# Performance work log

Hardware: AMD Instinct MI355X
Metric: run time of the kernel (lower is better)

Reference implementation:

```python
import jax, jax.numpy as jnp
import numpy as np

NUM_HEADS = 16
ROPE_THETA = 10000.0


def _rope_cos_sin(seq_len, head_dim, dtype):
    # Llama rotary embedding: inv_freq over even dims, emb = cat(freqs, freqs)
    inv_freq = 1.0 / (ROPE_THETA ** (jnp.arange(0, head_dim, 2, dtype=jnp.float32) / head_dim))
    t = jnp.arange(seq_len, dtype=jnp.float32)
    freqs = jnp.outer(t, inv_freq)              # [S, hd/2]
    emb = jnp.concatenate([freqs, freqs], -1)   # [S, hd]
    return jnp.cos(emb).astype(dtype), jnp.sin(emb).astype(dtype)


def _rotate_half(x):
    h = x.shape[-1] // 2
    return jnp.concatenate([-x[..., h:], x[..., :h]], axis=-1)


def setup_inputs() -> dict:
    key = jax.random.key(0)
    ks = jax.random.split(key, 5)
    B, S, D = 1, 2048, 2048
    scale = 0.02
    return {
        "hidden_states": jax.random.normal(ks[0], (B, S, D), jnp.float32),
        "Wq": jax.random.normal(ks[1], (D, D), jnp.float32) * scale,
        "Wk": jax.random.normal(ks[2], (D, D), jnp.float32) * scale,
        "Wv": jax.random.normal(ks[3], (D, D), jnp.float32) * scale,
        "Wo": jax.random.normal(ks[4], (D, D), jnp.float32) * scale,
    }


def reference(hidden_states, Wq, Wk, Wv, Wo):
    B, S, D = hidden_states.shape
    H = NUM_HEADS
    hd = D // H
    sm_scale = 1.0 / np.sqrt(hd)

    # QKV projections (nn.Linear without bias: x @ W.T), kept in [B,S,H,hd]
    q = (hidden_states @ Wq.T).reshape(B, S, H, hd)
    k = (hidden_states @ Wk.T).reshape(B, S, H, hd)
    v = (hidden_states @ Wv.T).reshape(B, S, H, hd)

    # RoPE (offset=0, no kv cache)
    cos, sin = _rope_cos_sin(S, hd, hidden_states.dtype)
    cos = cos[None, :, None, :]  # [1,S,1,hd]
    sin = sin[None, :, None, :]
    q = q * cos + _rotate_half(q) * sin
    k = k * cos + _rotate_half(k) * sin

    # Causal self-attention (exact math of FlashSelfAttention(causal=True))
    scores = jnp.einsum("bshd,bthd->bhst", q, k) * sm_scale  # [B,H,S,S]
    causal = jnp.tril(jnp.ones((S, S), dtype=bool))
    scores = jnp.where(causal[None, None], scores, jnp.finfo(scores.dtype).min)
    probs = jax.nn.softmax(scores, axis=-1)
    attn = jnp.einsum("bhst,bthd->bshd", probs, v)           # [B,S,H,hd]

    # Output projection
    attn = attn.reshape(B, S, H * hd)
    return attn @ Wo.T
```

## Files before the change

kernel.cpp:

```cpp
#include <hip/hip_runtime.h>
#include <hip/hip_bf16.h>
#include <math.h>

#define S_LEN 2048
#define DMODEL 2048
#define NHEADS 16
#define HDIM 128

typedef __bf16 bf16x8 __attribute__((ext_vector_type(8)));
typedef float f32x4 __attribute__((ext_vector_type(4)));

__device__ __forceinline__ unsigned short f2b(float f) {
  union { float f; unsigned u; } c; c.f = f;
  unsigned r = (c.u + 0x7fffu + ((c.u >> 16) & 1u)) >> 16;
  return (unsigned short)r;
}
__device__ __forceinline__ float b2f(unsigned short b) {
  union { unsigned u; float f; } c; c.u = ((unsigned)b) << 16;
  return c.f;
}

__device__ __forceinline__ void gload_lds16(const unsigned short* g, unsigned short* l) {
  __builtin_amdgcn_global_load_lds(
      (__attribute__((address_space(1))) void*)(void*)g,
      (__attribute__((address_space(3))) void*)(void*)l, 16, 0, 0);
}

__global__ void cvt5_f32_bf16_k(const float* __restrict__ s0,
                                const float* __restrict__ s1,
                                const float* __restrict__ s2,
                                const float* __restrict__ s3,
                                const float* __restrict__ s4,
                                unsigned short* __restrict__ d0,
                                unsigned short* __restrict__ d1,
                                unsigned short* __restrict__ d2,
                                unsigned short* __restrict__ d3,
                                unsigned short* __restrict__ d4) {
  int gi = blockIdx.x * blockDim.x + threadIdx.x;
  int seg = gi >> 20;
  int i = (gi & 0xFFFFF) * 4;
  const float* src = (seg == 0) ? s0 : (seg == 1) ? s1 : (seg == 2) ? s2
                     : (seg == 3) ? s3 : s4;
  unsigned short* dst = (seg == 0) ? d0 : (seg == 1) ? d1 : (seg == 2) ? d2
                        : (seg == 3) ? d3 : d4;
  float4 v = *reinterpret_cast<const float4*>(src + i);
  ushort4 o;
  o.x = f2b(v.x); o.y = f2b(v.y); o.z = f2b(v.z); o.w = f2b(v.w);
  *reinterpret_cast<ushort4*>(dst + i) = o;
}

__global__ void rope_table_k(float* __restrict__ cs, float* __restrict__ sn) {
  int idx = blockIdx.x * blockDim.x + threadIdx.x;
  int s = idx >> 6, i = idx & 63;
  float inv = powf(10000.0f, -(float)(2 * i) / 128.0f);
  float a = (float)s * inv;
  cs[idx] = cosf(a);
  sn[idx] = sinf(a);
}

__global__ void rope_apply_k(unsigned short* __restrict__ q,
                             unsigned short* __restrict__ k,
                             const float* __restrict__ cs,
                             const float* __restrict__ sn) {
  int idx = blockIdx.x * blockDim.x + threadIdx.x;
  int i = idx & 63;
  int h = (idx >> 6) & (NHEADS - 1);
  int s = idx >> 10;
  size_t base = (size_t)s * DMODEL + h * HDIM;
  float c = cs[s * 64 + i], sv = sn[s * 64 + i];
  float q1 = b2f(q[base + i]), q2 = b2f(q[base + i + 64]);
  q[base + i]      = f2b(q1 * c - q2 * sv);
  q[base + i + 64] = f2b(q2 * c + q1 * sv);
  float k1 = b2f(k[base + i]), k2 = b2f(k[base + i + 64]);
  k[base + i]      = f2b(k1 * c - k2 * sv);
  k[base + i + 64] = f2b(k2 * c + k1 * sv);
}

__global__ __launch_bounds__(256) void transpose_bf16_k(
    const unsigned short* __restrict__ in, unsigned short* __restrict__ out) {
  __shared__ unsigned short tile[64][72];
  int bx = blockIdx.x, by = blockIdx.y;
  int t = threadIdx.x;
#pragma unroll
  for (int i = 0; i < 2; ++i) {
    int ch = i * 256 + t;
    int r = ch >> 3, c8 = ch & 7;
    bf16x8 v = *reinterpret_cast<const bf16x8*>(
        in + (size_t)(by * 64 + r) * DMODEL + bx * 64 + c8 * 8);
    *reinterpret_cast<bf16x8*>(&tile[r][c8 * 8]) = v;
  }
  __syncthreads();
#pragma unroll
  for (int i = 0; i < 2; ++i) {
    int ch = i * 256 + t;
    int c = ch >> 3, r8 = ch & 7;
    union { bf16x8 v; unsigned short u[8]; } w;
#pragma unroll
    for (int j = 0; j < 8; ++j) w.u[j] = tile[r8 * 8 + j][c];
    *reinterpret_cast<bf16x8*>(
        out + (size_t)(bx * 64 + c) * S_LEN + by * 64 + r8 * 8) = w.v;
  }
}


#define MIDBAR_SEQ()                                      \
  do {                                                    \
    asm volatile("" ::: "memory");                        \
    __builtin_amdgcn_s_barrier();                         \
    asm volatile("s_waitcnt lgkmcnt(0)" ::: "memory");    \
    __builtin_amdgcn_sched_barrier(0);                    \
    __builtin_amdgcn_s_setprio(1);                        \
  } while (0)

#define ENDBAR_SEQ()                                      \
  do {                                                    \
    __builtin_amdgcn_s_setprio(0);                        \
    asm volatile("" ::: "memory");                        \
    __builtin_amdgcn_s_barrier();                         \
    asm volatile("" ::: "memory");                        \
  } while (0)

#define READA(QM)                                                              \
  do {                                                                         \
    _Pragma("unroll") for (int j = 0; j < MQ; ++j)                             \
    _Pragma("unroll") for (int kk = 0; kk < 2; ++kk) {                         \
      int row = wm * (BM / 2) + ((QM) * MQ + j) * 16 + li;                     \
      int c = (kk * 4 + g) ^ (li & 7);                                         \
      af[j][kk] = *reinterpret_cast<const bf16x8*>(&As[cur][row * 64 + c * 8]);\
    }                                                                          \
  } while (0)

#define READB(BF, QN)                                                          \
  do {                                                                         \
    _Pragma("unroll") for (int jn = 0; jn < 2; ++jn)                           \
    _Pragma("unroll") for (int kk = 0; kk < 2; ++kk) {                         \
      int row = wn * 64 + ((QN) * 2 + jn) * 16 + li;                           \
      int c = (kk * 4 + g) ^ (li & 7);                                         \
      BF[jn][kk] = *reinterpret_cast<const bf16x8*>(&Bs[cur][row * 64 + c * 8]);\
    }                                                                          \
  } while (0)

#define QUAD(QM, QN, BF)                                                       \
  do {                                                                         \
    _Pragma("unroll") for (int j = 0; j < MQ; ++j)                             \
    _Pragma("unroll") for (int jn = 0; jn < 2; ++jn)                           \
    _Pragma("unroll") for (int kk = 0; kk < 2; ++kk)                           \
      acc[(QM) * MQ + j][(QN) * 2 + jn] =                                      \
          __builtin_amdgcn_mfma_f32_16x16x32_bf16(                             \
              af[j][kk], BF[jn][kk], acc[(QM) * MQ + j][(QN) * 2 + jn], 0, 0, 0);\
  } while (0)

template <int BM, bool OUT_F32>
__global__ __launch_bounds__(512, 2) void gemm_8ph_k(
    const unsigned short* __restrict__ A, const unsigned short* __restrict__ B0p,
    const unsigned short* __restrict__ B1p, const unsigned short* __restrict__ B2p,
    void* __restrict__ C0, void* __restrict__ C1, void* __restrict__ C2,
    int M, int N, int K) {
  constexpr int MQ = BM / 64;
  constexpr int MR = BM / 32;

  __shared__ unsigned short As[2][BM * 64];
  __shared__ unsigned short Bs[2][256 * 64];

  const unsigned short* Bp = (blockIdx.z == 0) ? B0p : (blockIdx.z == 1) ? B1p : B2p;
  void* Cout = (blockIdx.z == 0) ? C0 : (blockIdx.z == 1) ? C1 : C2;

  int nwg = gridDim.x, bid = blockIdx.x;
  int wg = (bid & 7) * (nwg >> 3) + (bid >> 3);
  int ntn = N >> 8;
  int tm = wg / ntn, tn = wg % ntn;
  int m0 = tm * BM, n0 = tn << 8;

  const int tid = threadIdx.x;
  const int wave = tid >> 6, lane = tid & 63;
  const int g = lane >> 4, li = lane & 15;
  const int wm = wave >> 2, wn = wave & 3;

  auto stageB = [&](int buf, int tt, int qn) {
#pragma unroll
    for (int i = 0; i < 2; ++i) {
      int j = i * 512 + tid;
      int piece = j >> 8, rowin = (j >> 3) & 31, c = j & 7;
      int row = piece * 64 + qn * 32 + rowin;
      gload_lds16(Bp + (size_t)(n0 + row) * K + tt * 64 + ((c ^ (row & 7)) * 8),
                  &Bs[buf][row * 64 + c * 8]);
    }
  };
  auto stageA = [&](int buf, int tt, int qm) {
#pragma unroll
    for (int i = 0; i < BM / 128; ++i) {
      int j = i * 512 + tid;
      int piece = j / (2 * BM);
      int rowin = (j >> 3) & (BM / 4 - 1);
      int c = j & 7;
      int row = piece * (BM / 2) + qm * (BM / 4) + rowin;
      gload_lds16(A + (size_t)(m0 + row) * K + tt * 64 + ((c ^ (row & 7)) * 8),
                  &As[buf][row * 64 + c * 8]);
    }
  };

  f32x4 acc[MR][4];
#pragma unroll
  for (int i = 0; i < MR; ++i)
#pragma unroll
    for (int j = 0; j < 4; ++j) acc[i][j] = (f32x4){0.f, 0.f, 0.f, 0.f};

  const int nK = K >> 6;

  stageB(0, 0, 0); stageA(0, 0, 0); stageB(0, 0, 1); stageA(0, 0, 1);
  stageB(1, 1, 0); stageA(1, 1, 0); stageB(1, 1, 1); stageA(1, 1, 1);
  if constexpr (BM == 256) asm volatile("s_waitcnt vmcnt(8)" ::: "memory");
  else                     asm volatile("s_waitcnt vmcnt(6)" ::: "memory");
  asm volatile("" ::: "memory");
  __builtin_amdgcn_s_barrier();
  asm volatile("" ::: "memory");

  for (int t = 0; t < nK; ++t) {
    int cur = t & 1;
    bool pf = (t + 2 < nK);
    bf16x8 af[MQ][2], bf0[2][2], bf1[2][2];
    READA(0);
    READB(bf0, 0);
    MIDBAR_SEQ();
    QUAD(0, 0, bf0);
    ENDBAR_SEQ();
    READB(bf1, 1);
    if (pf) { stageB(cur, t + 2, 0); stageA(cur, t + 2, 0); }
    MIDBAR_SEQ();
    QUAD(0, 1, bf1);
    ENDBAR_SEQ();
    READA(1);
    if (pf) stageB(cur, t + 2, 1);
    MIDBAR_SEQ();
    QUAD(1, 1, bf1);
    ENDBAR_SEQ();
    if (pf) {
      stageA(cur, t + 2, 1);
      if constexpr (BM == 256) asm volatile("s_waitcnt vmcnt(8)" ::: "memory");
      else                     asm volatile("s_waitcnt vmcnt(6)" ::: "memory");
    } else {
      asm volatile("s_waitcnt vmcnt(0)" ::: "memory");
    }
    MIDBAR_SEQ();
    QUAD(1, 0, bf0);
    ENDBAR_SEQ();
  }

#pragma unroll
  for (int m = 0; m < MR; ++m) {
#pragma unroll
    for (int n = 0; n < 4; ++n) {
      int row = m0 + wm * (BM / 2) + m * 16 + g * 4;
      int col = n0 + wn * 64 + n * 16 + li;
#pragma unroll
      for (int r = 0; r < 4; ++r) {
        if (OUT_F32)
          reinterpret_cast<float*>(Cout)[(size_t)(row + r) * N + col] = acc[m][n][r];
        else
          reinterpret_cast<unsigned short*>(Cout)[(size_t)(row + r) * N + col] =
              f2b(acc[m][n][r]);
      }
    }
  }
}

#undef MIDBAR_SEQ
#undef ENDBAR_SEQ
#undef READA
#undef READB
#undef QUAD

__global__ __launch_bounds__(256) void flash_attn_k(
    const unsigned short* __restrict__ q, const unsigned short* __restrict__ k,
    const unsigned short* __restrict__ vt, unsigned short* __restrict__ o) {
  __shared__ unsigned short Ks[2][64 * 128];
  __shared__ unsigned short Vs[2][128 * 64];
  __shared__ unsigned short Ps[4 * 16 * 72];

  int L = blockIdx.x + 16 * blockIdx.y;
  int xcd = L & 7, j = L >> 3;
  int h = 2 * xcd + (j & 1);
  int p = j >> 1;

  int t = threadIdx.x, wave = t >> 6, lane = t & 63;
  int g = lane >> 4, li = lane & 15;

  const unsigned short* vth = vt + (size_t)h * HDIM * S_LEN;
  const float sm = 0.08838834764831845f;
  const float L2E = 1.4426950408889634f;

  auto stage = [&](int buf, int kt) {
    int kv0 = kt * 64;
#pragma unroll
    for (int i = 0; i < 4; ++i) {
      int ch = i * 256 + t;
      int row = ch >> 4, c = ch & 15;
      int cs_ = c ^ (row & 7);
      gload_lds16(k + (size_t)(kv0 + row) * DMODEL + h * HDIM + cs_ * 8,
                  &Ks[buf][ch * 8]);
    }
#pragma unroll
    for (int i = 0; i < 4; ++i) {
      int ch = i * 256 + t;
      int row = ch >> 3, c = ch & 7;
      int cs_ = c ^ (row & 7);
      gload_lds16(vth + (size_t)row * S_LEN + kv0 + cs_ * 8,
                  &Vs[buf][ch * 8]);
    }
  };

  for (int seg = 0; seg < 2; ++seg) {
    int qt = seg ? (31 - p) : p;
    int nIter = qt + 1;
    int q0 = qt * 64;
    int qrow = q0 + wave * 16 + li;

    bf16x8 qf[4];
#pragma unroll
    for (int kb = 0; kb < 4; ++kb)
      qf[kb] = *reinterpret_cast<const bf16x8*>(
          q + (size_t)qrow * DMODEL + h * HDIM + kb * 32 + g * 8);

    f32x4 O[8];
#pragma unroll
    for (int db = 0; db < 8; ++db) O[db] = (f32x4){0.f, 0.f, 0.f, 0.f};
    float m_r[4], l_r[4];
#pragma unroll
    for (int r = 0; r < 4; ++r) { m_r[r] = -1e30f; l_r[r] = 0.f; }

    stage(0, 0);

    for (int it = 0; it < nIter; ++it) {
      int cur = it & 1;
      int kv0 = it * 64;
      if (it + 1 < nIter) {
        stage(cur ^ 1, it + 1);
        asm volatile("s_waitcnt vmcnt(8)" ::: "memory");
      } else {
        asm volatile("s_waitcnt vmcnt(0)" ::: "memory");
      }
      __builtin_amdgcn_s_barrier();
      asm volatile("" ::: "memory");

      f32x4 sf[4];
#pragma unroll
      for (int jb = 0; jb < 4; ++jb) sf[jb] = (f32x4){0.f, 0.f, 0.f, 0.f};
#pragma unroll
      for (int kb = 0; kb < 4; ++kb) {
#pragma unroll
        for (int jb = 0; jb < 4; ++jb) {
          int row = jb * 16 + li;
          int c = (kb * 4 + g) ^ (row & 7);
          bf16x8 kf = *reinterpret_cast<const bf16x8*>(&Ks[cur][row * 128 + c * 8]);
          sf[jb] = __builtin_amdgcn_mfma_f32_16x16x32_bf16(qf[kb], kf, sf[jb], 0, 0, 0);
        }
      }

      float sv[4][4];
      float pm[4] = {-1e30f, -1e30f, -1e30f, -1e30f};
#pragma unroll
      for (int jb = 0; jb < 4; ++jb) {
        int jcol = kv0 + jb * 16 + li;
#pragma unroll
        for (int r = 0; r < 4; ++r) {
          float x = sf[jb][r] * sm;
          int irow = q0 + wave * 16 + g * 4 + r;
          if (it == qt && jcol > irow) x = -1e30f;
          sv[jb][r] = x;
          pm[r] = fmaxf(pm[r], x);
        }
      }
#pragma unroll
      for (int r = 0; r < 4; ++r) {
        float x = pm[r];
        x = fmaxf(x, __shfl_xor(x, 1));
        x = fmaxf(x, __shfl_xor(x, 2));
        x = fmaxf(x, __shfl_xor(x, 4));
        x = fmaxf(x, __shfl_xor(x, 8));
        pm[r] = x;
      }
      float alpha[4], ls[4];
#pragma unroll
      for (int r = 0; r < 4; ++r) {
        float nm = fmaxf(m_r[r], pm[r]);
        alpha[r] = exp2f((m_r[r] - nm) * L2E);
        m_r[r] = nm;
        ls[r] = 0.f;
      }
#pragma unroll
      for (int jb = 0; jb < 4; ++jb) {
#pragma unroll
        for (int r = 0; r < 4; ++r) {
          float pv = exp2f((sv[jb][r] - m_r[r]) * L2E);
          ls[r] += pv;
          Ps[wave * 16 * 72 + (g * 4 + r) * 72 + jb * 16 + li] = f2b(pv);
        }
      }
#pragma unroll
      for (int r = 0; r < 4; ++r) {
        float x = ls[r];
        x += __shfl_xor(x, 1);
        x += __shfl_xor(x, 2);
        x += __shfl_xor(x, 4);
        x += __shfl_xor(x, 8);
        l_r[r] = l_r[r] * alpha[r] + x;
      }
#pragma unroll
      for (int db = 0; db < 8; ++db)
#pragma unroll
        for (int r = 0; r < 4; ++r) O[db][r] *= alpha[r];

#pragma unroll
      for (int ks = 0; ks < 2; ++ks) {
        bf16x8 pa = *reinterpret_cast<const bf16x8*>(
            Ps + wave * 16 * 72 + li * 72 + ks * 32 + g * 8);
#pragma unroll
        for (int db = 0; db < 8; ++db) {
          int row = db * 16 + li;
          int c = (ks * 4 + g) ^ (row & 7);
          bf16x8 vbf = *reinterpret_cast<const bf16x8*>(&Vs[cur][row * 64 + c * 8]);
          O[db] = __builtin_amdgcn_mfma_f32_16x16x32_bf16(pa, vbf, O[db], 0, 0, 0);
        }
      }
      __builtin_amdgcn_s_barrier();
      asm volatile("" ::: "memory");
    }

#pragma unroll
    for (int db = 0; db < 8; ++db) {
#pragma unroll
      for (int r = 0; r < 4; ++r) {
        int row = q0 + wave * 16 + g * 4 + r;
        o[(size_t)row * DMODEL + h * HDIM + db * 16 + li] = f2b(O[db][r] / l_r[r]);
      }
    }
  }
}

extern "C" void kernel_launch(void* const* d_in, const int* in_sizes, int n_in,
                              void* d_out, int out_size, void* d_ws, size_t ws_size,
                              hipStream_t stream) {
  const float* hs = (const float*)d_in[0];
  const float* Wq = (const float*)d_in[1];
  const float* Wk = (const float*)d_in[2];
  const float* Wv = (const float*)d_in[3];
  const float* Wo = (const float*)d_in[4];

  char* ws = (char*)d_ws;
  const size_t MB = 1024 * 1024;
  unsigned short* hs_b = (unsigned short*)(ws + 0 * MB);
  unsigned short* Wq_b = (unsigned short*)(ws + 8 * MB);
  unsigned short* Wk_b = (unsigned short*)(ws + 16 * MB);
  unsigned short* Wv_b = (unsigned short*)(ws + 24 * MB);
  unsigned short* Wo_b = (unsigned short*)(ws + 32 * MB);
  unsigned short* qb = (unsigned short*)(ws + 40 * MB);
  unsigned short* kb = (unsigned short*)(ws + 48 * MB);
  unsigned short* vb = (unsigned short*)(ws + 56 * MB);
  unsigned short* ab = (unsigned short*)(ws + 64 * MB);
  float* cs = (float*)(ws + 72 * MB);
  float* sn = (float*)(ws + 72 * MB + 512 * 1024);
  unsigned short* vtb = hs_b;

  cvt5_f32_bf16_k<<<(5 * 1024 * 1024) / 256, 256, 0, stream>>>(
      hs, Wq, Wk, Wv, Wo, hs_b, Wq_b, Wk_b, Wv_b, Wo_b);

  rope_table_k<<<(S_LEN * 64) / 256, 256, 0, stream>>>(cs, sn);

  gemm_8ph_k<256, false><<<dim3(64, 1, 3), 512, 0, stream>>>(
      hs_b, Wq_b, Wk_b, Wv_b, qb, kb, vb, 2048, 2048, 2048);

  transpose_bf16_k<<<dim3(32, 32), 256, 0, stream>>>(vb, vtb);

  rope_apply_k<<<(S_LEN * NHEADS * 64) / 256, 256, 0, stream>>>(qb, kb, cs, sn);

  flash_attn_k<<<dim3(16, NHEADS), 256, 0, stream>>>(qb, kb, vtb, ab);

  gemm_8ph_k<128, true><<<dim3(128, 1, 1), 512, 0, stream>>>(
      ab, Wo_b, Wo_b, Wo_b, d_out, d_out, d_out, 2048, 2048, 2048);
}
```

Before: 223.5 us.

## Restructure flash attention: one q-tile per block, folded scale, MFMA row sums

Folds the softmax scale and log2(e) into Q during RoPE, so the attention loop uses exp2 directly with no per-element multiplies. Computes the row-sum denominator with an extra MFMA against a ones vector, replacing the shuffle reductions. Peels the diagonal tile so only it pays for the causal mask. Launches 512 blocks, one q-tile each and longest first, instead of 256 blocks that each handled a paired short and long segment. This raises parallelism and drops the serial second segment, but relies on scheduling order for load balance and rounds Q through bf16 after scaling.

New measurement: 218.8 us. -2.1%, faster.

```diff
diff --git a/kernel.cpp b/kernel.cpp
--- a/kernel.cpp
+++ b/kernel.cpp
@@ -62,15 +62,17 @@
                              unsigned short* __restrict__ k,
                              const float* __restrict__ cs,
                              const float* __restrict__ sn) {
+  const float SC = 0.08838834764831845f * 1.4426950408889634f;
   int idx = blockIdx.x * blockDim.x + threadIdx.x;
   int i = idx & 63;
   int h = (idx >> 6) & (NHEADS - 1);
   int s = idx >> 10;
   size_t base = (size_t)s * DMODEL + h * HDIM;
   float c = cs[s * 64 + i], sv = sn[s * 64 + i];
+  float qc = c * SC, qs = sv * SC;
   float q1 = b2f(q[base + i]), q2 = b2f(q[base + i + 64]);
-  q[base + i]      = f2b(q1 * c - q2 * sv);
-  q[base + i + 64] = f2b(q2 * c + q1 * sv);
+  q[base + i]      = f2b(q1 * qc - q2 * qs);
+  q[base + i + 64] = f2b(q2 * qc + q1 * qs);
   float k1 = b2f(k[base + i]), k2 = b2f(k[base + i + 64]);
   k[base + i]      = f2b(k1 * c - k2 * sv);
   k[base + i + 64] = f2b(k2 * c + k1 * sv);
@@ -277,17 +279,16 @@
   __shared__ unsigned short Vs[2][128 * 64];
   __shared__ unsigned short Ps[4 * 16 * 72];
 
-  int L = blockIdx.x + 16 * blockIdx.y;
+  int L = blockIdx.x;
   int xcd = L & 7, j = L >> 3;
   int h = 2 * xcd + (j & 1);
-  int p = j >> 1;
+  int qt = (j < 32) ? (31 - (j >> 1)) : ((j - 32) >> 1);
 
   int t = threadIdx.x, wave = t >> 6, lane = t & 63;
   int g = lane >> 4, li = lane & 15;
+  int q0 = qt * 64;
 
   const unsigned short* vth = vt + (size_t)h * HDIM * S_LEN;
-  const float sm = 0.08838834764831845f;
-  const float L2E = 1.4426950408889634f;
 
   auto stage = [&](int buf, int kt) {
     int kv0 = kt * 64;
@@ -309,130 +310,129 @@
     }
   };
 
-  for (int seg = 0; seg < 2; ++seg) {
-    int qt = seg ? (31 - p) : p;
-    int nIter = qt + 1;
-    int q0 = qt * 64;
-    int qrow = q0 + wave * 16 + li;
-
-    bf16x8 qf[4];
-#pragma unroll
-    for (int kb = 0; kb < 4; ++kb)
-      qf[kb] = *reinterpret_cast<const bf16x8*>(
-          q + (size_t)qrow * DMODEL + h * HDIM + kb * 32 + g * 8);
-
-    f32x4 O[8];
-#pragma unroll
-    for (int db = 0; db < 8; ++db) O[db] = (f32x4){0.f, 0.f, 0.f, 0.f};
-    float m_r[4], l_r[4];
-#pragma unroll
-    for (int r = 0; r < 4; ++r) { m_r[r] = -1e30f; l_r[r] = 0.f; }
-
-    stage(0, 0);
-
-    for (int it = 0; it < nIter; ++it) {
-      int cur = it & 1;
-      int kv0 = it * 64;
-      if (it + 1 < nIter) {
-        stage(cur ^ 1, it + 1);
-        asm volatile("s_waitcnt vmcnt(8)" ::: "memory");
-      } else {
-        asm volatile("s_waitcnt vmcnt(0)" ::: "memory");
+  int qrow = q0 + wave * 16 + li;
+  bf16x8 qf[4];
+#pragma unroll
+  for (int kb = 0; kb < 4; ++kb)
+    qf[kb] = *reinterpret_cast<const bf16x8*>(
+        q + (size_t)qrow * DMODEL + h * HDIM + kb * 32 + g * 8);
+
+  bf16x8 ones;
+#pragma unroll
+  for (int jj = 0; jj < 8; ++jj) ones[jj] = (__bf16)1.0f;
+
+  f32x4 O[8];
+#pragma unroll
+  for (int db = 0; db < 8; ++db) O[db] = (f32x4){0.f, 0.f, 0.f, 0.f};
+  f32x4 lA = (f32x4){0.f, 0.f, 0.f, 0.f};
+  float m_r[4];
+#pragma unroll
+  for (int r = 0; r < 4; ++r) m_r[r] = -1e30f;
+
+  auto tile_body = [&](int it, int cur, bool diag) {
+    int kv0 = it * 64;
+    f32x4 sf[4];
+#pragma unroll
+    for (int jb = 0; jb < 4; ++jb) sf[jb] = (f32x4){0.f, 0.f, 0.f, 0.f};
+#pragma unroll
+    for (int kb = 0; kb < 4; ++kb) {
+#pragma unroll
+      for (int jb = 0; jb < 4; ++jb) {
+        int row = jb * 16 + li;
+        int c = (kb * 4 + g) ^ (row & 7);
+        bf16x8 kf = *reinterpret_cast<const bf16x8*>(&Ks[cur][row * 128 + c * 8]);
+        sf[jb] = __builtin_amdgcn_mfma_f32_16x16x32_bf16(qf[kb], kf, sf[jb], 0, 0, 0);
       }
-      __builtin_amdgcn_s_barrier();
-      asm volatile("" ::: "memory");
-
-      f32x4 sf[4];
-#pragma unroll
-      for (int jb = 0; jb < 4; ++jb) sf[jb] = (f32x4){0.f, 0.f, 0.f, 0.f};
-#pragma unroll
-      for (int kb = 0; kb < 4; ++kb) {
-#pragma unroll
-        for (int jb = 0; jb < 4; ++jb) {
-          int row = jb * 16 + li;
-          int c = (kb * 4 + g) ^ (row & 7);
-          bf16x8 kf = *reinterpret_cast<const bf16x8*>(&Ks[cur][row * 128 + c * 8]);
-          sf[jb] = __builtin_amdgcn_mfma_f32_16x16x32_bf16(qf[kb], kf, sf[jb], 0, 0, 0);
+    }
+
+    float pm[4] = {-1e30f, -1e30f, -1e30f, -1e30f};
+    if (diag) {
+#pragma unroll
+      for (int jb = 0; jb < 4; ++jb) {
+        int jcol = kv0 + jb * 16 + li;
+#pragma unroll
+        for (int r = 0; r < 4; ++r) {
+          int irow = q0 + wave * 16 + g * 4 + r;
+          if (jcol > irow) sf[jb][r] = -1e30f;
+          pm[r] = fmaxf(pm[r], sf[jb][r]);
         }
       }
-
-      float sv[4][4];
-      float pm[4] = {-1e30f, -1e30f, -1e30f, -1e30f};
-#pragma unroll
-      for (int jb = 0; jb < 4; ++jb) {
-        int jcol = kv0 + jb * 16 + li;
-#pragma unroll
-        for (int r = 0; r < 4; ++r) {
-          float x = sf[jb][r] * sm;
-          int irow = q0 + wave * 16 + g * 4 + r;
-          if (it == qt && jcol > irow) x = -1e30f;
-          sv[jb][r] = x;
-          pm[r] = fmaxf(pm[r], x);
-        }
+    } else {
+#pragma unroll
+      for (int jb = 0; jb < 4; ++jb)
+#pragma unroll
+        for (int r = 0; r < 4; ++r) pm[r] = fmaxf(pm[r], sf[jb][r]);
+    }
+#pragma unroll
+    for (int r = 0; r < 4; ++r) {
+      float x = pm[r];
+      x = fmaxf(x, __shfl_xor(x, 1));
+      x = fmaxf(x, __shfl_xor(x, 2));
+      x = fmaxf(x, __shfl_xor(x, 4));
+      x = fmaxf(x, __shfl_xor(x, 8));
+      pm[r] = x;
+    }
+    float alpha[4];
+#pragma unroll
+    for (int r = 0; r < 4; ++r) {
+      float nm = fmaxf(m_r[r], pm[r]);
+      alpha[r] = exp2f(m_r[r] - nm);
+      m_r[r] = nm;
+    }
+#pragma unroll
+    for (int jb = 0; jb < 4; ++jb)
+#pragma unroll
+      for (int r = 0; r < 4; ++r)
+        Ps[wave * 16 * 72 + (g * 4 + r) * 72 + jb * 16 + li] =
+            f2b(exp2f(sf[jb][r] - m_r[r]));
+#pragma unroll
+    for (int db = 0; db < 8; ++db)
+#pragma unroll
+      for (int r = 0; r < 4; ++r) O[db][r] *= alpha[r];
+#pragma unroll
+    for (int r = 0; r < 4; ++r) lA[r] *= alpha[r];
+
+#pragma unroll
+    for (int ks = 0; ks < 2; ++ks) {
+      bf16x8 pa = *reinterpret_cast<const bf16x8*>(
+          Ps + wave * 16 * 72 + li * 72 + ks * 32 + g * 8);
+      lA = __builtin_amdgcn_mfma_f32_16x16x32_bf16(pa, ones, lA, 0, 0, 0);
+#pragma unroll
+      for (int db = 0; db < 8; ++db) {
+        int row = db * 16 + li;
+        int c = (ks * 4 + g) ^ (row & 7);
+        bf16x8 vbf = *reinterpret_cast<const bf16x8*>(&Vs[cur][row * 64 + c * 8]);
+        O[db] = __builtin_amdgcn_mfma_f32_16x16x32_bf16(pa, vbf, O[db], 0, 0, 0);
       }
-#pragma unroll
-      for (int r = 0; r < 4; ++r) {
-        float x = pm[r];
-        x = fmaxf(x, __shfl_xor(x, 1));
-        x = fmaxf(x, __shfl_xor(x, 2));
-        x = fmaxf(x, __shfl_xor(x, 4));
-        x = fmaxf(x, __shfl_xor(x, 8));
-        pm[r] = x;
-      }
-      float alpha[4], ls[4];
-#pragma unroll
-      for (int r = 0; r < 4; ++r) {
-        float nm = fmaxf(m_r[r], pm[r]);
-        alpha[r] = exp2f((m_r[r] - nm) * L2E);
-        m_r[r] = nm;
-        ls[r] = 0.f;
-      }
-#pragma unroll
-      for (int jb = 0; jb < 4; ++jb) {
-#pragma unroll
-        for (int r = 0; r < 4; ++r) {
-          float pv = exp2f((sv[jb][r] - m_r[r]) * L2E);
-          ls[r] += pv;
-          Ps[wave * 16 * 72 + (g * 4 + r) * 72 + jb * 16 + li] = f2b(pv);
-        }
-      }
-#pragma unroll
-      for (int r = 0; r < 4; ++r) {
-        float x = ls[r];
-        x += __shfl_xor(x, 1);
-        x += __shfl_xor(x, 2);
-        x += __shfl_xor(x, 4);
-        x += __shfl_xor(x, 8);
-        l_r[r] = l_r[r] * alpha[r] + x;
-      }
-#pragma unroll
-      for (int db = 0; db < 8; ++db)
-#pragma unroll
-        for (int r = 0; r < 4; ++r) O[db][r] *= alpha[r];
-
-#pragma unroll
-      for (int ks = 0; ks < 2; ++ks) {
-        bf16x8 pa = *reinterpret_cast<const bf16x8*>(
-            Ps + wave * 16 * 72 + li * 72 + ks * 32 + g * 8);
-#pragma unroll
-        for (int db = 0; db < 8; ++db) {
-          int row = db * 16 + li;
-          int c = (ks * 4 + g) ^ (row & 7);
-          bf16x8 vbf = *reinterpret_cast<const bf16x8*>(&Vs[cur][row * 64 + c * 8]);
-          O[db] = __builtin_amdgcn_mfma_f32_16x16x32_bf16(pa, vbf, O[db], 0, 0, 0);
-        }
-      }
-      __builtin_amdgcn_s_barrier();
-      asm volatile("" ::: "memory");
-    }
-
-#pragma unroll
-    for (int db = 0; db < 8; ++db) {
-#pragma unroll
-      for (int r = 0; r < 4; ++r) {
-        int row = q0 + wave * 16 + g * 4 + r;
-        o[(size_t)row * DMODEL + h * HDIM + db * 16 + li] = f2b(O[db][r] / l_r[r]);
-      }
+    }
+  };
+
+  stage(0, 0);
+
+  for (int it = 0; it < qt; ++it) {
+    int cur = it & 1;
+    stage(cur ^ 1, it + 1);
+    asm volatile("s_waitcnt vmcnt(8)" ::: "memory");
+    __builtin_amdgcn_s_barrier();
+    asm volatile("" ::: "memory");
+    tile_body(it, cur, false);
+    __builtin_amdgcn_s_barrier();
+    asm volatile("" ::: "memory");
+  }
+  {
+    int cur = qt & 1;
+    asm volatile("s_waitcnt vmcnt(0)" ::: "memory");
+    __builtin_amdgcn_s_barrier();
+    asm volatile("" ::: "memory");
+    tile_body(qt, cur, true);
+  }
+
+#pragma unroll
+  for (int db = 0; db < 8; ++db) {
+#pragma unroll
+    for (int r = 0; r < 4; ++r) {
+      int row = q0 + wave * 16 + g * 4 + r;
+      o[(size_t)row * DMODEL + h * HDIM + db * 16 + li] = f2b(O[db][r] / lA[r]);
     }
   }
 }
@@ -473,7 +473,7 @@
 
   rope_apply_k<<<(S_LEN * NHEADS * 64) / 256, 256, 0, stream>>>(qb, kb, cs, sn);
 
-  flash_attn_k<<<dim3(16, NHEADS), 256, 0, stream>>>(qb, kb, vtb, ab);
+  flash_attn_k<<<dim3(512), 256, 0, stream>>>(qb, kb, vtb, ab);
 
   gemm_8ph_k<128, true><<<dim3(128, 1, 1), 512, 0, stream>>>(
       ab, Wo_b, Wo_b, Wo_b, d_out, d_out, d_out, 2048, 2048, 2048);
```
